# Performance work log

Hardware: AMD Instinct MI355X
Metric: run time of the kernel (lower is better)

## Reference

```python
import jax, jax.numpy as jnp
import numpy as np

LAMBDA_TSA = 0.1
K = 25
P = 1
EPS = 1e-08


def setup_inputs() -> dict:
    key = jax.random.key(0)
    k1, k2, k3, k4 = jax.random.split(key, 4)
    B, D = 8192, 64
    return {
        "outputs": jax.random.normal(k1, (B, D), dtype=jnp.float32),
        "targets": jax.random.normal(k2, (B, D), dtype=jnp.float32),
        "latent": jax.random.normal(k3, (B, D), dtype=jnp.float32),
        "raw": jax.random.normal(k4, (B, D), dtype=jnp.float32),
    }


def _tsa_value(raw, latent):
    # raw, latent: [B, D]
    B, D = raw.shape
    # squared euclidean distances via gram trick (monotone in distance, so
    # topk-smallest indices match torch.cdist + topk(largest=False))
    sq = jnp.sum(raw * raw, axis=1)                      # [B]
    d2 = sq[:, None] + sq[None, :] - 2.0 * (raw @ raw.T)  # [B, B]
    _, idx = jax.lax.top_k(-d2, K + 1)                   # [B, K+1] nearest first
    nbrs = idx[:, 1:]                                    # [B, K] drop self

    Z = latent[nbrs]                                     # [B, K, D]
    X = raw[nbrs]                                        # [B, K, D]
    Zc = Z - jnp.mean(Z, axis=1, keepdims=True)
    Xc = X - jnp.mean(X, axis=1, keepdims=True)
    denom = K - 1 + EPS
    Cz = jnp.einsum('bkd,bke->bde', Zc, Zc) / denom       # [B, D, D]
    Cx = jnp.einsum('bkd,bke->bde', Xc, Xc) / denom       # [B, D, D]

    _, Uz = jnp.linalg.eigh(Cz)                          # ascending eigvals
    _, Ux = jnp.linalg.eigh(Cx)
    Ui = Uz[:, :, -P:]                                   # [B, D, P] top-P eigvecs
    Vi = Ux[:, :, -P:]
    Pz = jnp.einsum('bdp,bep->bde', Ui, Ui)              # projector [B, D, D]
    Px = jnp.einsum('bdp,bep->bde', Vi, Vi)
    per_sample = jnp.sum((Pz - Px) ** 2, axis=(1, 2))    # frobenius norm squared
    return jnp.mean(per_sample)


def reference(outputs, targets, latent, raw):
    recon = jnp.mean((outputs - targets) ** 2)
    # offload_cpu=True detaches raw/latent in the torch module
    raw_s = jax.lax.stop_gradient(raw)
    latent_s = jax.lax.stop_gradient(latent)
    tsa = LAMBDA_TSA * _tsa_value(raw_s, latent_s)
    return recon + tsa
```

## Files before the change

kernel.cpp:

```cpp
#include <hip/hip_runtime.h>
#include <hip/hip_bf16.h>


#define NB 8192
#define ND 64
#define KSEL 26
#define ROUNDS 12

__global__ __launch_bounds__(256) void tsa_sq_kernel(const float* __restrict__ raw,
                                                     float* __restrict__ sq,
                                                     float* __restrict__ reconS) {
    int row = blockIdx.x * 4 + (threadIdx.x >> 6);
    int lane = threadIdx.x & 63;
    float v = raw[row * 64 + lane];
    float s = v * v;
    #pragma unroll
    for (int off = 1; off < 64; off <<= 1) s += __shfl_xor(s, off);
    if (lane == 0) sq[row] = s;
    if (blockIdx.x == 0 && threadIdx.x == 0) reconS[0] = 0.0f;
}

__global__ __launch_bounds__(256) void tsa_transpose_kernel(const float* __restrict__ raw,
                                                            float* __restrict__ rawT) {
    __shared__ float tile[64][65];
    int t = threadIdx.x;
    int r0 = blockIdx.x * 64;
    #pragma unroll
    for (int r = 0; r < 4; ++r) {
        int e = r * 256 + t;
        int m = e >> 4, c4 = e & 15;
        float4 v = ((const float4*)raw)[(r0 + m) * 16 + c4];
        tile[m][c4 * 4 + 0] = v.x; tile[m][c4 * 4 + 1] = v.y;
        tile[m][c4 * 4 + 2] = v.z; tile[m][c4 * 4 + 3] = v.w;
    }
    __syncthreads();
    #pragma unroll
    for (int r = 0; r < 4; ++r) {
        int e = r * 256 + t;
        int k = e >> 4, c4 = e & 15;
        float4 v;
        v.x = tile[c4 * 4 + 0][k]; v.y = tile[c4 * 4 + 1][k];
        v.z = tile[c4 * 4 + 2][k]; v.w = tile[c4 * 4 + 3][k];
        ((float4*)rawT)[k * 2048 + (r0 >> 2) + c4] = v;
    }
}

__global__ __launch_bounds__(256) void tsa_recon_kernel(const float* __restrict__ o,
                                                        const float* __restrict__ tg,
                                                        float* __restrict__ reconS) {
    int idx = blockIdx.x * 256 + threadIdx.x;
    float4 a = ((const float4*)o)[idx];
    float4 b = ((const float4*)tg)[idx];
    float dx = a.x - b.x, dy = a.y - b.y, dz = a.z - b.z, dw = a.w - b.w;
    float s = dx * dx + dy * dy + dz * dz + dw * dw;
    #pragma unroll
    for (int off = 1; off < 64; off <<= 1) s += __shfl_xor(s, off);
    __shared__ float ps[4];
    if ((threadIdx.x & 63) == 0) ps[threadIdx.x >> 6] = s;
    __syncthreads();
    if (threadIdx.x == 0) atomicAdd(reconS, ps[0] + ps[1] + ps[2] + ps[3]);
}

__global__ __launch_bounds__(256) void tsa_dist_kernel(const float* __restrict__ rawT,
                                                       const float* __restrict__ sq,
                                                       float* __restrict__ d2,
                                                       int rowBase) {
    __shared__ float At[64 * 128];
    __shared__ float Bt[64 * 128];
    const int t = threadIdx.x;
    const int m0 = rowBase + blockIdx.y * 128;
    const int n0 = blockIdx.x * 128;
    const float4* rT4 = (const float4*)rawT;
    float4* At4 = (float4*)At;
    float4* Bt4 = (float4*)Bt;
    #pragma unroll
    for (int r = 0; r < 8; ++r) {
        int e = r * 256 + t;
        int k = e >> 5, c = e & 31;
        At4[e] = rT4[k * 2048 + (m0 >> 2) + c];
        Bt4[e] = rT4[k * 2048 + (n0 >> 2) + c];
    }
    __syncthreads();
    const int tx = t >> 4;
    const int ty = t & 15;
    float acc[8][8];
    #pragma unroll
    for (int i = 0; i < 8; ++i)
        #pragma unroll
        for (int j = 0; j < 8; ++j) acc[i][j] = 0.0f;

    #pragma unroll 4
    for (int k = 0; k < 64; ++k) {
        float4 a0 = At4[k * 32 + tx * 2 + 0];
        float4 a1 = At4[k * 32 + tx * 2 + 1];
        float4 b0 = Bt4[k * 32 + ty];
        float4 b1 = Bt4[k * 32 + 16 + ty];
        float av[8] = {a0.x, a0.y, a0.z, a0.w, a1.x, a1.y, a1.z, a1.w};
        float bw[8] = {b0.x, b0.y, b0.z, b0.w, b1.x, b1.y, b1.z, b1.w};
        #pragma unroll
        for (int i = 0; i < 8; ++i)
            #pragma unroll
            for (int j = 0; j < 8; ++j)
                acc[i][j] += av[i] * bw[j];
    }
    float sqm[8], sqn[8];
    #pragma unroll
    for (int i = 0; i < 8; ++i) sqm[i] = sq[m0 + tx * 8 + i];
    #pragma unroll
    for (int j = 0; j < 4; ++j) {
        sqn[j]     = sq[n0 + ty * 4 + j];
        sqn[4 + j] = sq[n0 + 64 + ty * 4 + j];
    }
    #pragma unroll
    for (int i = 0; i < 8; ++i) {
        size_t rowoff = (size_t)(m0 - rowBase + tx * 8 + i) * 8192;
        float4 w0, w1;
        w0.x = sqm[i] + sqn[0] - 2.0f * acc[i][0];
        w0.y = sqm[i] + sqn[1] - 2.0f * acc[i][1];
        w0.z = sqm[i] + sqn[2] - 2.0f * acc[i][2];
        w0.w = sqm[i] + sqn[3] - 2.0f * acc[i][3];
        w1.x = sqm[i] + sqn[4] - 2.0f * acc[i][4];
        w1.y = sqm[i] + sqn[5] - 2.0f * acc[i][5];
        w1.z = sqm[i] + sqn[6] - 2.0f * acc[i][6];
        w1.w = sqm[i] + sqn[7] - 2.0f * acc[i][7];
        float4* wp = (float4*)(d2 + rowoff + n0);
        wp[ty] = w0;
        wp[16 + ty] = w1;
    }
}

__global__ __launch_bounds__(256) void tsa_select_kernel(const float* __restrict__ d2,
                                                         int* __restrict__ nbrs,
                                                         int rowBase) {
    const int t = threadIdx.x;
    const int lane = t & 63;
    const int wv = t >> 6;
    const int i = rowBase + blockIdx.x;
    const float4* row4 = (const float4*)(d2 + (size_t)blockIdx.x * 8192u);

    float v[32];
    #pragma unroll
    for (int r = 0; r < 8; ++r) {
        float4 f = row4[wv * 512 + r * 64 + lane];
        v[4 * r + 0] = f.x; v[4 * r + 1] = f.y;
        v[4 * r + 2] = f.z; v[4 * r + 3] = f.w;
    }
    __shared__ float selV[4][KSEL];
    __shared__ int   selJ[4][KSEL];
    unsigned removed = 0;
    for (int round = 0; round < KSEL; ++round) {
        float bv = 3.0e38f; int bq = 0;
        #pragma unroll
        for (int q = 0; q < 32; ++q) {
            bool ok = ((removed >> q) & 1u) == 0u;
            bool c = ok && (v[q] < bv);
            bv = c ? v[q] : bv;
            bq = c ? q : bq;
        }
        int bj = wv * 2048 + (bq >> 2) * 256 + lane * 4 + (bq & 3);
        #pragma unroll
        for (int off = 1; off < 64; off <<= 1) {
            float rv = __shfl_xor(bv, off);
            int rj = __shfl_xor(bj, off);
            bool take = (rv < bv) || (rv == bv && rj < bj);
            bv = take ? rv : bv;
            bj = take ? rj : bj;
        }
        int jl = bj - wv * 2048;
        int ol = (jl >> 2) & 63;
        int oq = ((jl >> 8) << 2) | (jl & 3);
        if (lane == ol) removed |= (1u << oq);
        if (lane == 0) { selV[wv][round] = bv; selJ[wv][round] = bj; }
    }
    __syncthreads();
    if (wv == 0) {
        bool has = lane < 52;
        int p0 = lane, p1 = lane + 52;
        float v0 = has ? selV[p0 / KSEL][p0 % KSEL] : 3.0e38f;
        int   j0 = has ? selJ[p0 / KSEL][p0 % KSEL] : 0x7ffffffe;
        float v1 = has ? selV[p1 / KSEL][p1 % KSEL] : 3.0e38f;
        int   j1 = has ? selJ[p1 / KSEL][p1 % KSEL] : 0x7ffffffe;
        unsigned rm = 0;
        for (int round = 0; round < KSEL; ++round) {
            float bv = 3.0e38f; int bj = 0x7fffffff;
            if (!(rm & 1u)) { bv = v0; bj = j0; }
            if (!(rm & 2u) && (v1 < bv || (v1 == bv && j1 < bj))) { bv = v1; bj = j1; }
            #pragma unroll
            for (int off = 1; off < 64; off <<= 1) {
                float rv = __shfl_xor(bv, off);
                int rj = __shfl_xor(bj, off);
                bool take = (rv < bv) || (rv == bv && rj < bj);
                bv = take ? rv : bv;
                bj = take ? rj : bj;
            }
            if (bv == v0 && bj == j0) rm |= 1u;
            else if (bv == v1 && bj == j1) rm |= 2u;
            if (lane == 0 && round > 0) nbrs[i * 25 + round - 1] = bj;
        }
    }
}

__global__ __launch_bounds__(256) void tsa_eigen_kernel(const int* __restrict__ nbrs,
                                                        const float* __restrict__ latent,
                                                        const float* __restrict__ raw,
                                                        float* __restrict__ tsaV) {
    __shared__ float zx[4][2][25][68];
    __shared__ float gt[4][2][25][28];
    __shared__ float rsb[4][2][32];
    __shared__ int   jm_s[4][2];
    const int t = threadIdx.x, lane = t & 63, wv = t >> 6;
    const int i = blockIdx.x * 4 + wv;
    const int half = lane >> 5;
    const int b = lane & 31;
    const bool act = b < 25;
    const int bb = act ? b : 0;
    const float* src = half ? raw : latent;

    if (act) {
        int nb = nbrs[i * 25 + b];
        const float4* s4 = (const float4*)(src + nb * 64);
        float4* dst = (float4*)&zx[wv][half][b][0];
        #pragma unroll
        for (int c = 0; c < 16; ++c) dst[c] = s4[c];
    }
    __syncthreads();

    float g[25];
    #pragma unroll
    for (int a = 0; a < 25; ++a) g[a] = 0.0f;
    #pragma unroll 1
    for (int ch = 0; ch < 4; ++ch) {
        float ow[16];
        const float4* op = (const float4*)&zx[wv][half][bb][0];
        ((float4*)ow)[0] = op[ch * 4 + 0];
        ((float4*)ow)[1] = op[ch * 4 + 1];
        ((float4*)ow)[2] = op[ch * 4 + 2];
        ((float4*)ow)[3] = op[ch * 4 + 3];
        #pragma unroll
        for (int a = 0; a < 25; ++a) {
            float rr[16];
            const float4* rp = (const float4*)&zx[wv][half][a][0];
            ((float4*)rr)[0] = rp[ch * 4 + 0];
            ((float4*)rr)[1] = rp[ch * 4 + 1];
            ((float4*)rr)[2] = rp[ch * 4 + 2];
            ((float4*)rr)[3] = rp[ch * 4 + 3];
            float s = 0.0f;
            #pragma unroll
            for (int d4 = 0; d4 < 16; ++d4) s += ow[d4] * rr[d4];
            g[a] += s;
        }
    }

    {
        float rs_own = 0.0f;
        #pragma unroll
        for (int a = 0; a < 25; ++a) rs_own += g[a];
        if (act) rsb[wv][half][b] = rs_own;
        __syncthreads();
        float rsA[25];
        float grand = 0.0f;
        #pragma unroll
        for (int a = 0; a < 25; ++a) { rsA[a] = rsb[wv][half][a]; grand += rsA[a]; }
        const float c1 = 1.0f / 25.0f, c2 = 1.0f / 625.0f;
        #pragma unroll
        for (int a = 0; a < 25; ++a)
            g[a] = g[a] - rsA[a] * c1 - rs_own * c1 + grand * c2;
    }

    #pragma unroll 1
    for (int rd = 0; rd < ROUNDS; ++rd) {
        float ss = 0.0f;
        #pragma unroll
        for (int r2 = 0; r2 < 25; ++r2) ss += g[r2] * g[r2];
        ss = act ? ss : 0.0f;
        #pragma unroll
        for (int off = 1; off < 32; off <<= 1) ss += __shfl_xor(ss, off);
        float inv = 1.0f / ss;
        if (act) {
            float4* gw = (float4*)&gt[wv][half][b][0];
            gw[0] = make_float4(g[0], g[1], g[2], g[3]);
            gw[1] = make_float4(g[4], g[5], g[6], g[7]);
            gw[2] = make_float4(g[8], g[9], g[10], g[11]);
            gw[3] = make_float4(g[12], g[13], g[14], g[15]);
            gw[4] = make_float4(g[16], g[17], g[18], g[19]);
            gw[5] = make_float4(g[20], g[21], g[22], g[23]);
            gw[6] = make_float4(g[24], 0.0f, 0.0f, 0.0f);
        }
        __syncthreads();
        float ng[25];
        #pragma unroll
        for (int r2 = 0; r2 < 25; ++r2) ng[r2] = 0.0f;
        #pragma unroll
        for (int c = 0; c < 25; ++c) {
            float cc2[28];
            const float4* gr = (const float4*)&gt[wv][half][c][0];
            ((float4*)cc2)[0] = gr[0];
            ((float4*)cc2)[1] = gr[1];
            ((float4*)cc2)[2] = gr[2];
            ((float4*)cc2)[3] = gr[3];
            ((float4*)cc2)[4] = gr[4];
            ((float4*)cc2)[5] = gr[5];
            ((float4*)cc2)[6] = gr[6];
            float m2 = g[c];
            #pragma unroll
            for (int r2 = 0; r2 < 25; ++r2) ng[r2] += cc2[r2] * m2;
        }
        #pragma unroll
        for (int r2 = 0; r2 < 25; ++r2) g[r2] = ng[r2] * inv;
        __syncthreads();
    }

    if (act) {
        float4* gw = (float4*)&gt[wv][half][b][0];
        gw[0] = make_float4(g[0], g[1], g[2], g[3]);
        gw[1] = make_float4(g[4], g[5], g[6], g[7]);
        gw[2] = make_float4(g[8], g[9], g[10], g[11]);
        gw[3] = make_float4(g[12], g[13], g[14], g[15]);
        gw[4] = make_float4(g[16], g[17], g[18], g[19]);
        gw[5] = make_float4(g[20], g[21], g[22], g[23]);
        gw[6] = make_float4(g[24], 0.0f, 0.0f, 0.0f);
    }
    __syncthreads();

    float dv = act ? gt[wv][half][b][b] : -1.0f;
    int bi = b;
    #pragma unroll
    for (int off = 1; off < 32; off <<= 1) {
        float ov = __shfl_xor(dv, off);
        int oi = __shfl_xor(bi, off);
        bool take = (ov > dv) || (ov == dv && oi < bi);
        dv = take ? ov : dv;
        bi = take ? oi : bi;
    }
    if (lane == 0)  jm_s[wv][0] = bi;
    if (lane == 32) jm_s[wv][1] = bi;
    __syncthreads();
    int jz = jm_s[wv][0], jxm = jm_s[wv][1];

    float wzArr[28], wxArr[28];
    {
        const float4* wz4 = (const float4*)&gt[wv][0][jz][0];
        const float4* wx4 = (const float4*)&gt[wv][1][jxm][0];
        #pragma unroll
        for (int q = 0; q < 7; ++q) {
            ((float4*)wzArr)[q] = wz4[q];
            ((float4*)wxArr)[q] = wx4[q];
        }
    }
    float szs = 0.0f, sxs = 0.0f;
    #pragma unroll
    for (int k = 0; k < 25; ++k) { szs += wzArr[k]; sxs += wxArr[k]; }
    float azc = szs * (1.0f / 25.0f), axc = sxs * (1.0f / 25.0f);

    float uz = 0.0f, ux = 0.0f;
    #pragma unroll
    for (int k = 0; k < 25; ++k) {
        uz += zx[wv][0][k][lane] * (wzArr[k] - azc);
        ux += zx[wv][1][k][lane] * (wxArr[k] - axc);
    }
    float aa = uz * uz, bbv = ux * ux, ccv = uz * ux;
    #pragma unroll
    for (int off = 1; off < 64; off <<= 1) {
        aa += __shfl_xor(aa, off);
        bbv += __shfl_xor(bbv, off);
        ccv += __shfl_xor(ccv, off);
    }
    if (lane == 0) {
        float dot2 = (ccv * ccv) / fmaxf(aa * bbv, 1e-30f);
        tsaV[i] = 2.0f - 2.0f * dot2;
    }
}

__global__ __launch_bounds__(256) void tsa_final_kernel(const float* __restrict__ tsaV,
                                                        const float* __restrict__ reconS,
                                                        float* __restrict__ out) {
    float s = 0.0f;
    const float4* v4 = (const float4*)tsaV;
    for (int e = threadIdx.x; e < 2048; e += 256) {
        float4 v = v4[e];
        s += (v.x + v.y) + (v.z + v.w);
    }
    #pragma unroll
    for (int off = 1; off < 64; off <<= 1) s += __shfl_xor(s, off);
    __shared__ float ps[4];
    if ((threadIdx.x & 63) == 0) ps[threadIdx.x >> 6] = s;
    __syncthreads();
    if (threadIdx.x == 0) {
        float tot = ps[0] + ps[1] + ps[2] + ps[3];
        out[0] = reconS[0] * (1.0f / 524288.0f) + 0.1f * (tot * (1.0f / 8192.0f));
    }
}

extern "C" void kernel_launch(void* const* d_in, const int* in_sizes, int n_in,
                              void* d_out, int out_size, void* d_ws, size_t ws_size,
                              hipStream_t stream) {
    const float* outputs = (const float*)d_in[0];
    const float* targets = (const float*)d_in[1];
    const float* latent  = (const float*)d_in[2];
    const float* raw     = (const float*)d_in[3];

    float* ws = (float*)d_ws;
    float* sq     = ws;
    float* rawT   = ws + 8192;
    int*   nbrs   = (int*)(ws + 532480);
    float* reconS = ws + 737280;
    float* tsaV   = ws + 737296;
    float* d2buf  = ws + 745728;

    size_t availF = ws_size / 4;
    int R = 2048;
    while (R > 128 && (size_t)745728 + (size_t)R * 8192 > availF) R >>= 1;

    tsa_sq_kernel<<<2048, 256, 0, stream>>>(raw, sq, reconS);
    tsa_transpose_kernel<<<128, 256, 0, stream>>>(raw, rawT);
    tsa_recon_kernel<<<512, 256, 0, stream>>>(outputs, targets, reconS);

    for (int rb = 0; rb < 8192; rb += R) {
        dim3 g(64, R / 128);
        tsa_dist_kernel<<<g, 256, 0, stream>>>(rawT, sq, d2buf, rb);
        tsa_select_kernel<<<R, 256, 0, stream>>>(d2buf, nbrs, rb);
    }
    tsa_eigen_kernel<<<2048, 256, 0, stream>>>(nbrs, latent, raw, tsaV);
    tsa_final_kernel<<<1, 256, 0, stream>>>(tsaV, reconS, (float*)d_out);
}
```

Before: 758.0 us.

## Shrink eigen-kernel LDS via aliased per-wave pool, drop block barriers, fewer power rounds

Replaces the separate shared arrays with one per-half-wave pool. The Gram matrix scratch now overwrites the gathered neighbour rows, which cuts LDS per block and should allow more blocks per CU. Block-wide __syncthreads are replaced with LDS waitcnt fences and wave shuffles, since each wave only touches its own slice. The final projection re-reads neighbour rows from global memory instead of from LDS. Power-iteration rounds drop from 12 to 8, which risks less accurate top eigenvectors, and relying on waitcnt alone for intra-wave LDS ordering is fragile.

```diff
diff --git a/kernel.cpp b/kernel.cpp
--- a/kernel.cpp
+++ b/kernel.cpp
@@ -5,7 +5,7 @@
 #define NB 8192
 #define ND 64
 #define KSEL 26
-#define ROUNDS 12
+#define ROUNDS 8
 
 __global__ __launch_bounds__(256) void tsa_sq_kernel(const float* __restrict__ raw,
                                                      float* __restrict__ sq,
@@ -204,10 +204,7 @@
                                                         const float* __restrict__ latent,
                                                         const float* __restrict__ raw,
                                                         float* __restrict__ tsaV) {
-    __shared__ float zx[4][2][25][68];
-    __shared__ float gt[4][2][25][28];
-    __shared__ float rsb[4][2][32];
-    __shared__ int   jm_s[4][2];
+    __shared__ __align__(16) float pool[8][1700];
     const int t = threadIdx.x, lane = t & 63, wv = t >> 6;
     const int i = blockIdx.x * 4 + wv;
     const int half = lane >> 5;
@@ -215,15 +212,17 @@
     const bool act = b < 25;
     const int bb = act ? b : 0;
     const float* src = half ? raw : latent;
-
+    float* slice = pool[wv * 2 + half];
+
+    int nb = 0;
     if (act) {
-        int nb = nbrs[i * 25 + b];
+        nb = nbrs[i * 25 + b];
         const float4* s4 = (const float4*)(src + nb * 64);
-        float4* dst = (float4*)&zx[wv][half][b][0];
+        float4* dst = (float4*)(slice + b * 68);
         #pragma unroll
         for (int c = 0; c < 16; ++c) dst[c] = s4[c];
     }
-    __syncthreads();
+    asm volatile("s_waitcnt lgkmcnt(0)" ::: "memory");
 
     float g[25];
     #pragma unroll
@@ -231,7 +230,7 @@
     #pragma unroll 1
     for (int ch = 0; ch < 4; ++ch) {
         float ow[16];
-        const float4* op = (const float4*)&zx[wv][half][bb][0];
+        const float4* op = (const float4*)(slice + bb * 68);
         ((float4*)ow)[0] = op[ch * 4 + 0];
         ((float4*)ow)[1] = op[ch * 4 + 1];
         ((float4*)ow)[2] = op[ch * 4 + 2];
@@ -239,7 +238,7 @@
         #pragma unroll
         for (int a = 0; a < 25; ++a) {
             float rr[16];
-            const float4* rp = (const float4*)&zx[wv][half][a][0];
+            const float4* rp = (const float4*)(slice + a * 68);
             ((float4*)rr)[0] = rp[ch * 4 + 0];
             ((float4*)rr)[1] = rp[ch * 4 + 1];
             ((float4*)rr)[2] = rp[ch * 4 + 2];
@@ -255,12 +254,13 @@
         float rs_own = 0.0f;
         #pragma unroll
         for (int a = 0; a < 25; ++a) rs_own += g[a];
-        if (act) rsb[wv][half][b] = rs_own;
-        __syncthreads();
+        float grand = 0.0f;
         float rsA[25];
-        float grand = 0.0f;
-        #pragma unroll
-        for (int a = 0; a < 25; ++a) { rsA[a] = rsb[wv][half][a]; grand += rsA[a]; }
+        #pragma unroll
+        for (int a = 0; a < 25; ++a) {
+            rsA[a] = __shfl(rs_own, half * 32 + a);
+            grand += rsA[a];
+        }
         const float c1 = 1.0f / 25.0f, c2 = 1.0f / 625.0f;
         #pragma unroll
         for (int a = 0; a < 25; ++a)
@@ -277,7 +277,7 @@
         for (int off = 1; off < 32; off <<= 1) ss += __shfl_xor(ss, off);
         float inv = 1.0f / ss;
         if (act) {
-            float4* gw = (float4*)&gt[wv][half][b][0];
+            float4* gw = (float4*)(slice + b * 28);
             gw[0] = make_float4(g[0], g[1], g[2], g[3]);
             gw[1] = make_float4(g[4], g[5], g[6], g[7]);
             gw[2] = make_float4(g[8], g[9], g[10], g[11]);
@@ -286,14 +286,14 @@
             gw[5] = make_float4(g[20], g[21], g[22], g[23]);
             gw[6] = make_float4(g[24], 0.0f, 0.0f, 0.0f);
         }
-        __syncthreads();
+        asm volatile("s_waitcnt lgkmcnt(0)" ::: "memory");
         float ng[25];
         #pragma unroll
         for (int r2 = 0; r2 < 25; ++r2) ng[r2] = 0.0f;
         #pragma unroll
         for (int c = 0; c < 25; ++c) {
             float cc2[28];
-            const float4* gr = (const float4*)&gt[wv][half][c][0];
+            const float4* gr = (const float4*)(slice + c * 28);
             ((float4*)cc2)[0] = gr[0];
             ((float4*)cc2)[1] = gr[1];
             ((float4*)cc2)[2] = gr[2];
@@ -307,11 +307,10 @@
         }
         #pragma unroll
         for (int r2 = 0; r2 < 25; ++r2) g[r2] = ng[r2] * inv;
-        __syncthreads();
     }
 
     if (act) {
-        float4* gw = (float4*)&gt[wv][half][b][0];
+        float4* gw = (float4*)(slice + b * 28);
         gw[0] = make_float4(g[0], g[1], g[2], g[3]);
         gw[1] = make_float4(g[4], g[5], g[6], g[7]);
         gw[2] = make_float4(g[8], g[9], g[10], g[11]);
@@ -320,9 +319,9 @@
         gw[5] = make_float4(g[20], g[21], g[22], g[23]);
         gw[6] = make_float4(g[24], 0.0f, 0.0f, 0.0f);
     }
-    __syncthreads();
-
-    float dv = act ? gt[wv][half][b][b] : -1.0f;
+    asm volatile("s_waitcnt lgkmcnt(0)" ::: "memory");
+
+    float dv = act ? slice[b * 28 + b] : -1.0f;
     int bi = b;
     #pragma unroll
     for (int off = 1; off < 32; off <<= 1) {
@@ -332,15 +331,15 @@
         dv = take ? ov : dv;
         bi = take ? oi : bi;
     }
-    if (lane == 0)  jm_s[wv][0] = bi;
-    if (lane == 32) jm_s[wv][1] = bi;
-    __syncthreads();
-    int jz = jm_s[wv][0], jxm = jm_s[wv][1];
-
+    int jz = __shfl(bi, 0);
+    int jxm = __shfl(bi, 32);
+
+    const float* slice0 = pool[wv * 2 + 0];
+    const float* slice1 = pool[wv * 2 + 1];
     float wzArr[28], wxArr[28];
     {
-        const float4* wz4 = (const float4*)&gt[wv][0][jz][0];
-        const float4* wx4 = (const float4*)&gt[wv][1][jxm][0];
+        const float4* wz4 = (const float4*)(slice0 + jz * 28);
+        const float4* wx4 = (const float4*)(slice1 + jxm * 28);
         #pragma unroll
         for (int q = 0; q < 7; ++q) {
             ((float4*)wzArr)[q] = wz4[q];
@@ -355,8 +354,10 @@
     float uz = 0.0f, ux = 0.0f;
     #pragma unroll
     for (int k = 0; k < 25; ++k) {
-        uz += zx[wv][0][k][lane] * (wzArr[k] - azc);
-        ux += zx[wv][1][k][lane] * (wxArr[k] - axc);
+        int nbz = __shfl(nb, k);
+        int nbx = __shfl(nb, 32 + k);
+        uz += latent[nbz * 64 + lane] * (wzArr[k] - azc);
+        ux += raw[nbx * 64 + lane] * (wxArr[k] - axc);
     }
     float aa = uz * uz, bbv = ux * ux, ccv = uz * ux;
     #pragma unroll
```

New measurement: 739.6 us. -2.4%, faster.
